# Performance work log

Hardware: AMD Instinct MI355X
Metric: run time of the kernel (lower is better)

Reference implementation:

```python
import jax, jax.numpy as jnp
import numpy as np

N = 50000   # nodes per domain graph
E = 800000  # edges per graph (avg degree 16)
IN = 512    # in_feats
H = 256     # n_hidden
C = 10      # n_classes
ALPHA = 1.0


def setup_inputs() -> dict:
    key = jax.random.key(0)
    ks = jax.random.split(key, 16)
    inp = {
        "features_s": jax.random.normal(ks[0], (N, IN), jnp.float32),
        "labels_s": jax.random.randint(ks[1], (N,), 0, C, jnp.int32),
        "features_t": jax.random.normal(ks[2], (N, IN), jnp.float32),
        "src_s": jax.random.randint(ks[3], (E,), 0, N, jnp.int32),
        "dst_s": jax.random.randint(ks[4], (E,), 0, N, jnp.int32),
        "src_t": jax.random.randint(ks[5], (E,), 0, N, jnp.int32),
        "dst_t": jax.random.randint(ks[6], (E,), 0, N, jnp.int32),
        # GraphConv layer 0: in_feats -> n_hidden (glorot-ish init)
        "W0": jax.random.normal(ks[7], (IN, H), jnp.float32) / np.float32(np.sqrt(IN)),
        "b0": jnp.zeros((H,), jnp.float32),
        # GraphConv layer 1: n_hidden -> n_hidden
        "W1": jax.random.normal(ks[8], (H, H), jnp.float32) / np.float32(np.sqrt(H)),
        "b1": jnp.zeros((H,), jnp.float32),
        # fc head: n_hidden -> n_classes
        "Wfc": jax.random.normal(ks[9], (H, C), jnp.float32) / np.float32(np.sqrt(H)),
        "bfc": jnp.zeros((C,), jnp.float32),
        # JS discriminator: (n_hidden*n_layers + n_classes) -> 2
        "Wd": jax.random.normal(ks[10], (H * 2 + C, 2), jnp.float32) / np.float32(np.sqrt(H * 2 + C)),
        "bd": jnp.zeros((2,), jnp.float32),
    }
    return inp


def _gconv(x, src, dst, W, b, n):
    # DGL GraphConv with norm='both': out = D_in^{-1/2} A D_out^{-1/2} x W + b, then relu.
    ones = jnp.ones(src.shape, x.dtype)
    deg_out = jax.ops.segment_sum(ones, src, num_segments=n)
    deg_in = jax.ops.segment_sum(ones, dst, num_segments=n)
    norm_src = jnp.maximum(deg_out, 1.0) ** -0.5   # [n]
    norm_dst = jnp.maximum(deg_in, 1.0) ** -0.5    # [n]
    h = (x * norm_src[:, None]) @ W                # [n, out] (mult-first: row scaling commutes)
    agg = jax.ops.segment_sum(h[src], dst, num_segments=n)  # gather-scatter SpMM
    return jax.nn.relu(agg * norm_dst[:, None] + b)


def reference(features_s, labels_s, features_t, src_s, dst_s, src_t, dst_t,
              W0, b0, W1, b1, Wfc, bfc, Wd, bd):
    # dropout omitted (eval-mode determinism)
    hs, ht = features_s, features_t
    s_list, t_list = [], []
    for (W, b) in ((W0, b0), (W1, b1)):
        hs = _gconv(hs, src_s, dst_s, W, b, N)
        ht = _gconv(ht, src_t, dst_t, W, b, N)
        s_list.append(hs)
        t_list.append(ht)
    logits_s = hs @ Wfc + bfc
    logits_t = ht @ Wfc + bfc
    s_list.append(logits_s)
    t_list.append(logits_t)

    # class loss: nll over log_softmax
    logp = jax.nn.log_softmax(logits_s, axis=-1)
    class_loss = -jnp.mean(jnp.take_along_axis(logp, labels_s[:, None].astype(jnp.int32), axis=1))

    # JS domain loss with gradient-reversal (identity in forward)
    s_f = jnp.concatenate(s_list, axis=1)  # [N, 2H+C]
    t_f = jnp.concatenate(t_list, axis=1)
    both = jnp.concatenate([s_f, t_f], axis=0)  # [2N, 2H+C]
    rev = -ALPHA * both + jax.lax.stop_gradient((1.0 + ALPHA) * both)  # GRL trick
    dlogits = rev @ Wd + bd
    dlogp = jax.nn.log_softmax(dlogits, axis=-1)
    dlabels = jnp.concatenate([jnp.zeros((N,), jnp.int32), jnp.ones((N,), jnp.int32)])
    domain_loss = -jnp.mean(jnp.take_along_axis(dlogp, dlabels[:, None], axis=1))

    return class_loss + 0.01 * domain_loss
```

## Files before the change

kernel.cpp:

```cpp
#include <hip/hip_runtime.h>
#include <cstdint>
#include <cstddef>

#define NN 50000
#define NNP 50016
#define EE 800000
#define INF 512
#define HH  256
#define CC  10
#define NB2 391
#define NTB 782
#define SPMM_BLOCKS 1600
#define NFB 104
#define PSZ 12500
#define HBIN 6250
#define HRNG 8
#define HSUB 32
#define SCAP 1536
#define ZROW NN

using bfrag = __attribute__((ext_vector_type(8))) __bf16;
using f32x4 = __attribute__((ext_vector_type(4))) float;

__device__ inline unsigned short f2bf(float x) {
    unsigned u = __builtin_bit_cast(unsigned, x);
    unsigned r = u + 0x7FFFu + ((u >> 16) & 1u);
    return (unsigned short)(r >> 16);
}
__device__ inline float bf2f(unsigned short h) {
    return __builtin_bit_cast(float, (unsigned)h << 16);
}

__device__ inline void gload_lds16(const void* gsrc, void* ldst) {
    __builtin_amdgcn_global_load_lds(
        (const __attribute__((address_space(1))) void*)gsrc,
        (__attribute__((address_space(3))) void*)ldst, 16, 0, 0);
}

template<int K>
__global__ void k_cast_wt(const float* __restrict__ W, ushort* __restrict__ Wt) {
    int idx = blockIdx.x * blockDim.x + threadIdx.x;
    if (idx >= K * HH) return;
    int n = idx / K, k = idx % K;
    Wt[idx] = f2bf(W[(size_t)k * HH + n]);
}

__global__ void k_cast_wtail(const float* __restrict__ Wfc, const float* __restrict__ Wd,
                             ushort* __restrict__ Wt1) {
    int idx = blockIdx.x * blockDim.x + threadIdx.x;
    if (idx >= 16 * HH) return;
    int n = idx >> 8, k = idx & 255;
    float v = 0.f;
    if (n < 10)       v = Wfc[(size_t)k * 10 + n];
    else if (n < 12)  v = Wd[(size_t)(HH + k) * 2 + (n - 10)];
    Wt1[idx] = f2bf(v);
}

__global__ void k_cast_wtail2(const float* __restrict__ Wd, ushort* __restrict__ Wt2) {
    int idx = blockIdx.x * blockDim.x + threadIdx.x;
    if (idx >= 16 * HH) return;
    int n = idx >> 8, k = idx & 255;
    float v = (n < 2) ? Wd[(size_t)k * 2 + n] : 0.f;
    Wt2[idx] = f2bf(v);
}

__global__ __launch_bounds__(256) void k_deghist(
        const int* __restrict__ src_s, const int* __restrict__ dst_s,
        const int* __restrict__ src_t, const int* __restrict__ dst_t,
        ushort* __restrict__ pcnt) {
    __shared__ int hist[HBIN];
    const int task = blockIdx.x >> 5;
    const int sub  = blockIdx.x & 31;
    const int arr = task >> 3, range = task & 7;
    const int* p = (arr == 0) ? src_s : (arr == 1) ? dst_s : (arr == 2) ? src_t : dst_t;
    const int4* p4 = reinterpret_cast<const int4*>(p);
    const int lo = range * HBIN;
    for (int j = threadIdx.x; j < HBIN; j += 256) hist[j] = 0;
    __syncthreads();
    for (int i = sub * 256 + (int)threadIdx.x; i < EE / 4; i += HSUB * 256) {
        int4 v = p4[i];
        int a0 = v.x - lo, a1 = v.y - lo, a2 = v.z - lo, a3 = v.w - lo;
        if ((unsigned)a0 < (unsigned)HBIN) atomicAdd(&hist[a0], 1);
        if ((unsigned)a1 < (unsigned)HBIN) atomicAdd(&hist[a1], 1);
        if ((unsigned)a2 < (unsigned)HBIN) atomicAdd(&hist[a2], 1);
        if ((unsigned)a3 < (unsigned)HBIN) atomicAdd(&hist[a3], 1);
    }
    __syncthreads();
    ushort* out = pcnt + ((size_t)task * HSUB + sub) * HBIN;
    for (int j = threadIdx.x; j < HBIN; j += 256) out[j] = (ushort)hist[j];
}

__global__ void k_degsum(const ushort* __restrict__ pcnt, int* __restrict__ cnt) {
    int g = blockIdx.x * blockDim.x + threadIdx.x;
    if (g >= 4 * NN) return;
    int arr = g / NN;
    int node = g - arr * NN;
    int range = node / HBIN;
    int j = node - range * HBIN;
    const ushort* p = pcnt + ((size_t)(arr * HRNG + range) * HSUB) * HBIN + j;
    int s = 0;
    #pragma unroll
    for (int k = 0; k < HSUB; ++k) s += p[(size_t)k * HBIN];
    cnt[g] = s;
}

__global__ void k_scan_blk(const int* __restrict__ cnt, int* __restrict__ off,
                           int* __restrict__ btot) {
    __shared__ int wsum[4];
    int tid = threadIdx.x, lane = tid & 63, wid = tid >> 6;
    int i = blockIdx.x * 256 + tid;
    int v = 0;
    if (i < 2 * NN) v = (i < NN) ? cnt[NN + i] : cnt[2 * NN + i];
    int s = v;
    #pragma unroll
    for (int o = 1; o < 64; o <<= 1) {
        int t = __shfl_up(s, o, 64);
        if (lane >= o) s += t;
    }
    if (lane == 63) wsum[wid] = s;
    __syncthreads();
    if (tid == 0) {
        int a = 0;
        #pragma unroll
        for (int w2 = 0; w2 < 4; ++w2) { int t = wsum[w2]; wsum[w2] = a; a += t; }
        btot[blockIdx.x] = a;
    }
    __syncthreads();
    if (i < 2 * NN) off[i] = wsum[wid] + s - v;
}

__global__ void k_scan_tops(const int* __restrict__ btot, int* __restrict__ bbase,
                            int* __restrict__ off) {
    __shared__ int wsum[8];
    int tid = threadIdx.x, lane = tid & 63, wid = tid >> 6;
    int v = (tid < NB2) ? btot[tid] : 0;
    int s = v;
    #pragma unroll
    for (int o = 1; o < 64; o <<= 1) {
        int t = __shfl_up(s, o, 64);
        if (lane >= o) s += t;
    }
    if (lane == 63) wsum[wid] = s;
    __syncthreads();
    if (tid == 0) {
        int a = 0;
        #pragma unroll
        for (int w2 = 0; w2 < 8; ++w2) { int t = wsum[w2]; wsum[w2] = a; a += t; }
        off[2 * NN] = a;
    }
    __syncthreads();
    if (tid < NB2) bbase[tid] = wsum[wid] + s - v;
}

__global__ void k_scan_fin(int* __restrict__ off, const int* __restrict__ bbase,
                           int* __restrict__ cur, const int* __restrict__ cnt,
                           float* __restrict__ ns, float* __restrict__ nd,
                           ushort* __restrict__ y2) {
    if (blockIdx.x == 0 && threadIdx.x < 256) {
        int g = threadIdx.x >> 5, c = threadIdx.x & 31;
        y2[((size_t)g * NNP + ZROW) * 32 + c] = 0;
    }
    int i = blockIdx.x * blockDim.x + threadIdx.x;
    if (i >= 2 * NN) return;
    int o = off[i] + bbase[i >> 8];
    off[i] = o;
    cur[i] = o;
    int co = (i < NN) ? cnt[i] : cnt[NN + i];
    int ci = (i < NN) ? cnt[NN + i] : cnt[2 * NN + i];
    ns[i] = 1.0f / sqrtf(fmaxf((float)co, 1.0f));
    nd[i] = 1.0f / sqrtf(fmaxf((float)ci, 1.0f));
}

__global__ __launch_bounds__(256) void k_fill_part(
        const int* __restrict__ src_s, const int* __restrict__ dst_s,
        const int* __restrict__ src_t, const int* __restrict__ dst_t,
        int* __restrict__ cur, int* __restrict__ csr_src) {
    const int p = blockIdx.x & 7;
    const int blk = blockIdx.x >> 3;
    const unsigned lo = p * PSZ;
    for (int e = blk * 256 + (int)threadIdx.x; e < 2 * EE; e += NFB * 256) {
        int node;
        if (e < EE) node = dst_s[e];
        else        node = NN + dst_t[e - EE];
        if ((unsigned)(node - lo) < (unsigned)PSZ) {
            int sv = (e < EE) ? src_s[e] : src_t[e - EE];
            int pos = atomicAdd(&cur[node], 1);
            csr_src[pos] = sv;
        }
    }
}

template<int K, bool F32A>
__global__ __launch_bounds__(256, 2) void k_gemm(
        const void* __restrict__ Ap, const ushort* __restrict__ Bt,
        const float* __restrict__ ns, ushort* __restrict__ y2) {
    __shared__ ushort As[128 * 64];
    __shared__ ushort Bs[256 * 64];
    const int m0 = blockIdx.x * 128;
    const int t = threadIdx.x;
    const int wid = t >> 6, lane = t & 63;
    const int wr = (wid & 1) * 64;
    const int wc = (wid >> 1) * 128;
    const int l15 = lane & 15, lg = lane >> 4;

    f32x4 acc[4][8];
    #pragma unroll
    for (int m = 0; m < 4; ++m)
        #pragma unroll
        for (int n = 0; n < 8; ++n)
            acc[m][n] = {0.f, 0.f, 0.f, 0.f};

    const int srow = t >> 3;
    const int schunk = t & 7;

    for (int k0 = 0; k0 < K; k0 += 64) {
        if constexpr (F32A) {
            #pragma unroll
            for (int i = 0; i < 4; ++i) {
                int row = srow + i * 32;
                int sw = ((schunk ^ (row & 7)) * 8);
                int m = m0 + row; if (m >= NN) m = NN - 1;
                const float* ap = (const float*)Ap + (size_t)m * K + k0 + schunk * 8;
                float4 f0 = *reinterpret_cast<const float4*>(ap);
                float4 f1 = *reinterpret_cast<const float4*>(ap + 4);
                uint4 va;
                va.x = (unsigned)f2bf(f0.x) | ((unsigned)f2bf(f0.y) << 16);
                va.y = (unsigned)f2bf(f0.z) | ((unsigned)f2bf(f0.w) << 16);
                va.z = (unsigned)f2bf(f1.x) | ((unsigned)f2bf(f1.y) << 16);
                va.w = (unsigned)f2bf(f1.z) | ((unsigned)f2bf(f1.w) << 16);
                *reinterpret_cast<uint4*>(&As[row * 64 + sw]) = va;
            }
        } else {
            #pragma unroll
            for (int i = 0; i < 4; ++i) {
                int row = srow + i * 32;
                int sw = ((schunk ^ (row & 7)) * 8);
                int m = m0 + row; if (m >= NN) m = NN - 1;
                const ushort* gsrc = (const ushort*)Ap + (size_t)m * K + k0 + sw;
                gload_lds16(gsrc, &As[(size_t)(wid * 8 + i * 32) * 64]);
            }
        }
        #pragma unroll
        for (int i = 0; i < 8; ++i) {
            int row = srow + i * 32;
            int sw = ((schunk ^ (row & 7)) * 8);
            const ushort* gsrc = &Bt[(size_t)row * K + k0 + sw];
            gload_lds16(gsrc, &Bs[(size_t)(wid * 8 + i * 32) * 64]);
        }
        __syncthreads();
        #pragma unroll
        for (int kk = 0; kk < 64; kk += 32) {
            const int kc = kk >> 3;
            bfrag af[4];
            #pragma unroll
            for (int m = 0; m < 4; ++m) {
                int row = wr + m * 16 + l15;
                af[m] = *reinterpret_cast<const bfrag*>(&As[row * 64 + (((lg + kc) ^ (row & 7)) * 8)]);
            }
            #pragma unroll
            for (int n = 0; n < 8; ++n) {
                int row = wc + n * 16 + l15;
                bfrag bg = *reinterpret_cast<const bfrag*>(&Bs[row * 64 + (((lg + kc) ^ (row & 7)) * 8)]);
                #pragma unroll
                for (int m = 0; m < 4; ++m)
                    acc[m][n] = __builtin_amdgcn_mfma_f32_16x16x32_bf16(af[m], bg, acc[m][n], 0, 0, 0);
            }
        }
        __syncthreads();
    }
    #pragma unroll
    for (int m = 0; m < 4; ++m) {
        #pragma unroll
        for (int r = 0; r < 4; ++r) {
            int row = m0 + wr + m * 16 + lg * 4 + r;
            if (row >= NN) continue;
            float nsv = ns[row];
            #pragma unroll
            for (int n = 0; n < 8; ++n) {
                int col = wc + n * 16 + l15;
                int grp = col >> 5, colw = col & 31;
                y2[((size_t)grp * NNP + row) * 32 + colw] = f2bf(acc[m][n][r] * nsv);
            }
        }
    }
}

__device__ inline void add8(float* a, uint4 v) {
    a[0] += __builtin_bit_cast(float, v.x << 16);
    a[1] += __builtin_bit_cast(float, v.x & 0xffff0000u);
    a[2] += __builtin_bit_cast(float, v.y << 16);
    a[3] += __builtin_bit_cast(float, v.y & 0xffff0000u);
    a[4] += __builtin_bit_cast(float, v.z << 16);
    a[5] += __builtin_bit_cast(float, v.z & 0xffff0000u);
    a[6] += __builtin_bit_cast(float, v.w << 16);
    a[7] += __builtin_bit_cast(float, v.w & 0xffff0000u);
}

__global__ __launch_bounds__(256) void k_spmm6(
        const ushort* __restrict__ y2, const int* __restrict__ off,
        const int* __restrict__ csr_src, const float* __restrict__ nd_arr,
        const float* __restrict__ bias, ushort* __restrict__ h_out) {
    __shared__ int sidx[4][SCAP];
    const int grp = blockIdx.x & 7;
    const int blk = blockIdx.x >> 3;
    const int tid = threadIdx.x;
    const int lane = tid & 63, wid = tid >> 6;
    const int slot = lane >> 2;
    const int sub = lane & 3;
    const ushort* ybase = y2 + (size_t)grp * NNP * 32 + sub * 8;

    const int nb = (blk * 4 + wid) * 64;
    int s_wave0 = 0, cnt = 0;
    if (nb < NN) {
        int nend = nb + 64 < NN ? nb + 64 : NN;
        s_wave0 = off[nb];
        cnt = off[nend] - s_wave0;
    }
    int stage = cnt < SCAP ? cnt : SCAP;
    for (int j = lane; j < stage; j += 64)
        sidx[wid][j] = csr_src[s_wave0 + j];
    __syncthreads();

    float bia[8];
    #pragma unroll
    for (int j = 0; j < 8; ++j) bia[j] = bias[grp * 32 + sub * 8 + j];

    int e0[4], e1[4];
    float a[4][8];
    #pragma unroll
    for (int c = 0; c < 4; ++c) {
        int n = nb + c * 16 + slot;
        bool v = n < NN;
        e0[c] = v ? off[n] - s_wave0 : 0;
        e1[c] = v ? off[n + 1] - s_wave0 : 0;
        #pragma unroll
        for (int j = 0; j < 8; ++j) a[c][j] = 0.f;
    }
    int tmax = max(max(e1[0] - e0[0], e1[1] - e0[1]), max(e1[2] - e0[2], e1[3] - e0[3]));

    if (cnt <= SCAP) {
        for (int t = 0; t < tmax; ++t) {
            uint4 v[4];
            #pragma unroll
            for (int c = 0; c < 4; ++c) {
                int ec = e0[c] + t;
                bool val = ec < e1[c];
                int ecc = val ? ec : 0;
                int id = sidx[wid][ecc];
                id = val ? id : ZROW;
                v[c] = *reinterpret_cast<const uint4*>(&ybase[(size_t)id * 32]);
            }
            #pragma unroll
            for (int c = 0; c < 4; ++c) add8(a[c], v[c]);
        }
    } else {
        for (int t = 0; t < tmax; ++t) {
            uint4 v[4];
            #pragma unroll
            for (int c = 0; c < 4; ++c) {
                int ec = e0[c] + t;
                bool val = ec < e1[c];
                int ecc = val ? ec : 0;
                int id = csr_src[s_wave0 + ecc];
                id = val ? id : ZROW;
                v[c] = *reinterpret_cast<const uint4*>(&ybase[(size_t)id * 32]);
            }
            #pragma unroll
            for (int c = 0; c < 4; ++c) add8(a[c], v[c]);
        }
    }

    #pragma unroll
    for (int c = 0; c < 4; ++c) {
        int n = nb + c * 16 + slot;
        if (n >= NN) continue;
        float nd = nd_arr[n];
        ushort r[8];
        #pragma unroll
        for (int j = 0; j < 8; ++j) r[j] = f2bf(fmaxf(a[c][j] * nd + bia[j], 0.f));
        uint4 pk;
        pk.x = (unsigned)r[0] | ((unsigned)r[1] << 16);
        pk.y = (unsigned)r[2] | ((unsigned)r[3] << 16);
        pk.z = (unsigned)r[4] | ((unsigned)r[5] << 16);
        pk.w = (unsigned)r[6] | ((unsigned)r[7] << 16);
        *reinterpret_cast<uint4*>(&h_out[(size_t)n * 256 + grp * 32 + sub * 8]) = pk;
    }
}

__global__ __launch_bounds__(256) void k_tail_mfma(
        const ushort* __restrict__ h0, const ushort* __restrict__ h1,
        const ushort* __restrict__ Wt1, const ushort* __restrict__ Wt2,
        const float* __restrict__ bfc, const float* __restrict__ bd,
        const int* __restrict__ labels, int g,
        float* __restrict__ pcls, float* __restrict__ pdom) {
    __shared__ float sT1[4][16][17];
    __shared__ float sT2[4][16][17];
    __shared__ float sc[4], sd[4];
    const int tid = threadIdx.x;
    const int wid = tid >> 6, lane = tid & 63;
    const int l15 = lane & 15, lg = lane >> 4;
    const int base = blockIdx.x * 64 + wid * 16;

    int arow = base + l15; if (arow >= NN) arow = NN - 1;
    const ushort* a1 = h1 + (size_t)arow * 256 + lg * 8;
    const ushort* a0 = h0 + (size_t)arow * 256 + lg * 8;
    const ushort* b1 = Wt1 + (size_t)l15 * 256 + lg * 8;
    const ushort* b2 = Wt2 + (size_t)l15 * 256 + lg * 8;
    f32x4 acc1 = {0.f, 0.f, 0.f, 0.f};
    f32x4 acc2 = {0.f, 0.f, 0.f, 0.f};
    #pragma unroll
    for (int kk = 0; kk < 8; ++kk) {
        bfrag af1 = *reinterpret_cast<const bfrag*>(a1 + kk * 32);
        bfrag bg1 = *reinterpret_cast<const bfrag*>(b1 + kk * 32);
        acc1 = __builtin_amdgcn_mfma_f32_16x16x32_bf16(af1, bg1, acc1, 0, 0, 0);
        bfrag af0 = *reinterpret_cast<const bfrag*>(a0 + kk * 32);
        bfrag bg2 = *reinterpret_cast<const bfrag*>(b2 + kk * 32);
        acc2 = __builtin_amdgcn_mfma_f32_16x16x32_bf16(af0, bg2, acc2, 0, 0, 0);
    }
    #pragma unroll
    for (int j = 0; j < 4; ++j) {
        sT1[wid][lg * 4 + j][l15] = acc1[j];
        sT2[wid][lg * 4 + j][l15] = acc2[j];
    }
    __syncthreads();

    float cls = 0.f, dom = 0.f;
    int n = base + lane;
    if (lane < 16 && n < NN) {
        float lgt[10];
        #pragma unroll
        for (int c = 0; c < 10; ++c) lgt[c] = sT1[wid][lane][c] + bfc[c];
        float dl0 = bd[0] + sT2[wid][lane][0] + sT1[wid][lane][10];
        float dl1 = bd[1] + sT2[wid][lane][1] + sT1[wid][lane][11];
        if (g == 0) {
            float m = lgt[0];
            #pragma unroll
            for (int c = 1; c < 10; ++c) m = fmaxf(m, lgt[c]);
            float s = 0.f;
            #pragma unroll
            for (int c = 0; c < 10; ++c) s += expf(lgt[c] - m);
            int lab = labels[n];
            float tgt = lgt[0];
            #pragma unroll
            for (int c = 1; c < 10; ++c) tgt = (c == lab) ? lgt[c] : tgt;
            cls = -(tgt - (m + logf(s)));
        }
        float m2 = fmaxf(dl0, dl1);
        float lse2 = m2 + logf(expf(dl0 - m2) + expf(dl1 - m2));
        dom = -((g ? dl1 : dl0) - lse2);
    }
    #pragma unroll
    for (int o = 1; o < 16; o <<= 1) {
        cls += __shfl_xor(cls, o, 64);
        dom += __shfl_xor(dom, o, 64);
    }
    if (lane == 0) { sc[wid] = cls; sd[wid] = dom; }
    __syncthreads();
    if (tid == 0) {
        float c = sc[0] + sc[1] + sc[2] + sc[3];
        float d = sd[0] + sd[1] + sd[2] + sd[3];
        if (g == 0) pcls[blockIdx.x] = c;
        pdom[g * NTB + blockIdx.x] = d;
    }
}

__global__ void k_finalize(const float* __restrict__ pcls, const float* __restrict__ pdom,
                           float* __restrict__ out) {
    __shared__ float sc[4], sd[4];
    int tid = threadIdx.x, lane = tid & 63, wid = tid >> 6;
    float c = 0.f, d = 0.f;
    for (int i = tid; i < NTB; i += 256) c += pcls[i];
    for (int i = tid; i < 2 * NTB; i += 256) d += pdom[i];
    #pragma unroll
    for (int o = 32; o; o >>= 1) {
        c += __shfl_xor(c, o, 64);
        d += __shfl_xor(d, o, 64);
    }
    if (lane == 0) { sc[wid] = c; sd[wid] = d; }
    __syncthreads();
    if (tid == 0) {
        float ct = sc[0] + sc[1] + sc[2] + sc[3];
        float dt = sd[0] + sd[1] + sd[2] + sd[3];
        out[0] = ct / (float)NN + 0.01f * (dt / (float)(2 * NN));
    }
}

extern "C" void kernel_launch(void* const* d_in, const int* in_sizes, int n_in,
                              void* d_out, int out_size, void* d_ws, size_t ws_size,
                              hipStream_t stream) {
    const float* features_s = (const float*)d_in[0];
    const int*   labels_s   = (const int*)d_in[1];
    const float* features_t = (const float*)d_in[2];
    const int*   src_s      = (const int*)d_in[3];
    const int*   dst_s      = (const int*)d_in[4];
    const int*   src_t      = (const int*)d_in[5];
    const int*   dst_t      = (const int*)d_in[6];
    const float* W0         = (const float*)d_in[7];
    const float* b0         = (const float*)d_in[8];
    const float* W1         = (const float*)d_in[9];
    const float* b1         = (const float*)d_in[10];
    const float* Wfc        = (const float*)d_in[11];
    const float* bfc        = (const float*)d_in[12];
    const float* Wd         = (const float*)d_in[13];
    const float* bd         = (const float*)d_in[14];
    float* out = (float*)d_out;

    auto align256 = [](size_t x) { return (x + 255) & ~(size_t)255; };
    char* w = (char*)d_ws;
    ushort* h0     = (ushort*)w; w += align256((size_t)NN * HH * 2);
    ushort* h1     = (ushort*)w; w += align256((size_t)NN * HH * 2);
    ushort* y2     = (ushort*)w; w += align256((size_t)NNP * HH * 2);
    ushort* W0t    = (ushort*)w; w += align256((size_t)INF * HH * 2);
    ushort* W1t    = (ushort*)w; w += align256((size_t)HH * HH * 2);
    ushort* Wt1    = (ushort*)w; w += align256((size_t)16 * HH * 2);
    ushort* Wt2    = (ushort*)w; w += align256((size_t)16 * HH * 2);
    float* ns      = (float*)w;  w += align256((size_t)2 * NN * 4);
    float* nd      = (float*)w;  w += align256((size_t)2 * NN * 4);
    int*   cnt     = (int*)w;    w += align256((size_t)4 * NN * 4);
    int*   csr_off = (int*)w;    w += align256((size_t)(2 * NN + 1) * 4);
    int*   csr_cur = (int*)w;    w += align256((size_t)2 * NN * 4);
    int*   csr_src = (int*)w;    w += align256((size_t)2 * EE * 4);
    int*   btot    = (int*)w;    w += align256((size_t)NB2 * 4);
    int*   bbase   = (int*)w;    w += align256((size_t)NB2 * 4);
    float* pcls    = (float*)w;  w += align256((size_t)NTB * 4);
    float* pdom    = (float*)w;  w += align256((size_t)2 * NTB * 4);
    ushort* pcnt   = (ushort*)w; w += align256((size_t)4 * HRNG * HSUB * HBIN * 2);

    const int TB = 256;
    k_cast_wt<INF><<<(INF * HH + TB - 1) / TB, TB, 0, stream>>>(W0, W0t);
    k_cast_wt<HH><<<(HH * HH + TB - 1) / TB, TB, 0, stream>>>(W1, W1t);
    k_cast_wtail<<<(16 * HH + TB - 1) / TB, TB, 0, stream>>>(Wfc, Wd, Wt1);
    k_cast_wtail2<<<(16 * HH + TB - 1) / TB, TB, 0, stream>>>(Wd, Wt2);

    k_deghist<<<4 * HRNG * HSUB, TB, 0, stream>>>(src_s, dst_s, src_t, dst_t, pcnt);
    k_degsum<<<(4 * NN + TB - 1) / TB, TB, 0, stream>>>(pcnt, cnt);
    k_scan_blk<<<NB2, TB, 0, stream>>>(cnt, csr_off, btot);
    k_scan_tops<<<1, 512, 0, stream>>>(btot, bbase, csr_off);
    k_scan_fin<<<NB2, TB, 0, stream>>>(csr_off, bbase, csr_cur, cnt, ns, nd, y2);
    k_fill_part<<<NFB * 8, TB, 0, stream>>>(src_s, dst_s, src_t, dst_t,
                                            csr_cur, csr_src);

    const int GB = (NN + 127) / 128;
    for (int g = 0; g < 2; ++g) {
        const float* feats = g ? features_t : features_s;
        const int*   offg  = csr_off + (size_t)g * NN;
        const float* nsg   = ns + (size_t)g * NN;
        const float* ndg   = nd + (size_t)g * NN;

        k_gemm<INF, true><<<GB, TB, 0, stream>>>(feats, W0t, nsg, y2);
        k_spmm6<<<SPMM_BLOCKS, TB, 0, stream>>>(y2, offg, csr_src, ndg, b0, h0);
        k_gemm<HH, false><<<GB, TB, 0, stream>>>(h0, W1t, nsg, y2);
        k_spmm6<<<SPMM_BLOCKS, TB, 0, stream>>>(y2, offg, csr_src, ndg, b1, h1);
        k_tail_mfma<<<NTB, TB, 0, stream>>>(h0, h1, Wt1, Wt2, bfc, bd, labels_s, g,
                                            pcls, pdom);
    }
    k_finalize<<<1, TB, 0, stream>>>(pcls, pdom, out);
}
```

Baseline: 474.1 us.

## Fill CSR with LDS-local cursors from per-subchunk histogram prefix offsets

Replaces the global-atomic CSR fill with a two-step scheme. A new kernel turns the existing per-subchunk degree histograms into per-(range, subchunk) starting offsets. The fill kernel then keeps cursors for one node range in shared memory and uses LDS atomics while reading dst as int4. This removes contended global atomics on the cursor array and the repeated full scans across 8 partitions. In exchange it adds a base-offset buffer and an extra kernel, and it relies on the fill kernel's edge-to-subchunk striding matching the histogram kernel's striding.

```diff
diff --git a/kernel.cpp b/kernel.cpp
--- a/kernel.cpp
+++ b/kernel.cpp
@@ -11,8 +11,6 @@
 #define NB2 391
 #define NTB 782
 #define SPMM_BLOCKS 1600
-#define NFB 104
-#define PSZ 12500
 #define HBIN 6250
 #define HRNG 8
 #define HSUB 32
@@ -153,7 +151,7 @@
 }
 
 __global__ void k_scan_fin(int* __restrict__ off, const int* __restrict__ bbase,
-                           int* __restrict__ cur, const int* __restrict__ cnt,
+                           const int* __restrict__ cnt,
                            float* __restrict__ ns, float* __restrict__ nd,
                            ushort* __restrict__ y2) {
     if (blockIdx.x == 0 && threadIdx.x < 256) {
@@ -164,28 +162,58 @@
     if (i >= 2 * NN) return;
     int o = off[i] + bbase[i >> 8];
     off[i] = o;
-    cur[i] = o;
     int co = (i < NN) ? cnt[i] : cnt[NN + i];
     int ci = (i < NN) ? cnt[NN + i] : cnt[2 * NN + i];
     ns[i] = 1.0f / sqrtf(fmaxf((float)co, 1.0f));
     nd[i] = 1.0f / sqrtf(fmaxf((float)ci, 1.0f));
 }
 
-__global__ __launch_bounds__(256) void k_fill_part(
+__global__ void k_degpos(const ushort* __restrict__ pcnt, const int* __restrict__ off,
+                         int* __restrict__ base2) {
+    int i = blockIdx.x * blockDim.x + threadIdx.x;
+    if (i >= 2 * NN) return;
+    int g = (i < NN) ? 0 : 1;
+    int node = i - g * NN;
+    int range = node / HBIN;
+    int bin = node - range * HBIN;
+    int arr = g ? 3 : 1;
+    const ushort* p = pcnt + ((size_t)(arr * HRNG + range) * HSUB) * HBIN + bin;
+    int* b = base2 + ((size_t)(g * HRNG + range) * HSUB) * HBIN + bin;
+    int run = off[i];
+    #pragma unroll
+    for (int s = 0; s < HSUB; ++s) {
+        b[(size_t)s * HBIN] = run;
+        run += p[(size_t)s * HBIN];
+    }
+}
+
+__global__ __launch_bounds__(256) void k_fill3(
         const int* __restrict__ src_s, const int* __restrict__ dst_s,
         const int* __restrict__ src_t, const int* __restrict__ dst_t,
-        int* __restrict__ cur, int* __restrict__ csr_src) {
-    const int p = blockIdx.x & 7;
-    const int blk = blockIdx.x >> 3;
-    const unsigned lo = p * PSZ;
-    for (int e = blk * 256 + (int)threadIdx.x; e < 2 * EE; e += NFB * 256) {
-        int node;
-        if (e < EE) node = dst_s[e];
-        else        node = NN + dst_t[e - EE];
-        if ((unsigned)(node - lo) < (unsigned)PSZ) {
-            int sv = (e < EE) ? src_s[e] : src_t[e - EE];
-            int pos = atomicAdd(&cur[node], 1);
-            csr_src[pos] = sv;
+        const int* __restrict__ base2, int* __restrict__ csr_src) {
+    __shared__ int cur[HBIN];
+    const int combo = blockIdx.x & 15;
+    const int sub = blockIdx.x >> 4;
+    const int g = combo >> 3, range = combo & 7;
+    const int4* d4 = reinterpret_cast<const int4*>(g ? dst_t : dst_s);
+    const int4* s4 = reinterpret_cast<const int4*>(g ? src_t : src_s);
+    const int lo = range * HBIN;
+    const int* b = base2 + (size_t)combo * HSUB * HBIN + (size_t)sub * HBIN;
+    for (int j = threadIdx.x; j < HBIN; j += 256) cur[j] = b[j];
+    __syncthreads();
+    for (int i = sub * 256 + (int)threadIdx.x; i < EE / 4; i += HSUB * 256) {
+        int4 d = d4[i];
+        int b0 = d.x - lo, b1 = d.y - lo, b2 = d.z - lo, b3 = d.w - lo;
+        bool o0 = (unsigned)b0 < (unsigned)HBIN;
+        bool o1 = (unsigned)b1 < (unsigned)HBIN;
+        bool o2 = (unsigned)b2 < (unsigned)HBIN;
+        bool o3 = (unsigned)b3 < (unsigned)HBIN;
+        if (o0 | o1 | o2 | o3) {
+            int4 s = s4[i];
+            if (o0) csr_src[atomicAdd(&cur[b0], 1)] = s.x;
+            if (o1) csr_src[atomicAdd(&cur[b1], 1)] = s.y;
+            if (o2) csr_src[atomicAdd(&cur[b2], 1)] = s.z;
+            if (o3) csr_src[atomicAdd(&cur[b3], 1)] = s.w;
         }
     }
 }
@@ -518,13 +546,13 @@
     float* nd      = (float*)w;  w += align256((size_t)2 * NN * 4);
     int*   cnt     = (int*)w;    w += align256((size_t)4 * NN * 4);
     int*   csr_off = (int*)w;    w += align256((size_t)(2 * NN + 1) * 4);
-    int*   csr_cur = (int*)w;    w += align256((size_t)2 * NN * 4);
     int*   csr_src = (int*)w;    w += align256((size_t)2 * EE * 4);
     int*   btot    = (int*)w;    w += align256((size_t)NB2 * 4);
     int*   bbase   = (int*)w;    w += align256((size_t)NB2 * 4);
     float* pcls    = (float*)w;  w += align256((size_t)NTB * 4);
     float* pdom    = (float*)w;  w += align256((size_t)2 * NTB * 4);
     ushort* pcnt   = (ushort*)w; w += align256((size_t)4 * HRNG * HSUB * HBIN * 2);
+    int*   base2   = (int*)w;    w += align256((size_t)2 * HRNG * HSUB * HBIN * 4);
 
     const int TB = 256;
     k_cast_wt<INF><<<(INF * HH + TB - 1) / TB, TB, 0, stream>>>(W0, W0t);
@@ -536,9 +564,9 @@
     k_degsum<<<(4 * NN + TB - 1) / TB, TB, 0, stream>>>(pcnt, cnt);
     k_scan_blk<<<NB2, TB, 0, stream>>>(cnt, csr_off, btot);
     k_scan_tops<<<1, 512, 0, stream>>>(btot, bbase, csr_off);
-    k_scan_fin<<<NB2, TB, 0, stream>>>(csr_off, bbase, csr_cur, cnt, ns, nd, y2);
-    k_fill_part<<<NFB * 8, TB, 0, stream>>>(src_s, dst_s, src_t, dst_t,
-                                            csr_cur, csr_src);
+    k_scan_fin<<<NB2, TB, 0, stream>>>(csr_off, bbase, cnt, ns, nd, y2);
+    k_degpos<<<NB2, TB, 0, stream>>>(pcnt, csr_off, base2);
+    k_fill3<<<16 * HSUB, TB, 0, stream>>>(src_s, dst_s, src_t, dst_t, base2, csr_src);
 
     const int GB = (NN + 127) / 128;
     for (int g = 0; g < 2; ++g) {
```

New measurement: 443.5 us. 6.5% less time.
